# Optimization experiments

Hardware: AMD Instinct MI355X
Metric: run time of the kernel (lower is better)

Reference implementation:

```python
import jax, jax.numpy as jnp
import numpy as np

H = 2048      # hidden_size
NH = 16       # num_heads
HD = H // NH  # head_dim
B, T = 2, 2048


def setup_inputs() -> dict:
    key = jax.random.key(0)
    ks = jax.random.split(key, 5)
    s = 1.0 / np.sqrt(H)
    return {
        "x": jax.random.normal(ks[0], (B, T, H), dtype=jnp.float32),
        "wq": jax.random.normal(ks[1], (H, H), dtype=jnp.float32) * s,
        "bq": jnp.zeros((H,), dtype=jnp.float32),
        "wk": jax.random.normal(ks[2], (H, H), dtype=jnp.float32) * s,
        "bk": jnp.zeros((H,), dtype=jnp.float32),
        "wv": jax.random.normal(ks[3], (H, H), dtype=jnp.float32) * s,
        "bv": jnp.zeros((H,), dtype=jnp.float32),
        "wo": jax.random.normal(ks[4], (H, H), dtype=jnp.float32) * s,
        "bo": jnp.zeros((H,), dtype=jnp.float32),
    }


def reference(x, wq, bq, wk, bk, wv, bv, wo, bo):
    Bx, Tx, C = x.shape
    # projections (torch Linear: x @ W.T + b)
    q = x @ wq.T + bq
    k = x @ wk.T + bk
    v = x @ wv.T + bv
    # [B, T, H] -> [B, NH, T, HD]
    q = q.reshape(Bx, Tx, NH, HD).transpose(0, 2, 1, 3)
    k = k.reshape(Bx, Tx, NH, HD).transpose(0, 2, 1, 3)
    v = v.reshape(Bx, Tx, NH, HD).transpose(0, 2, 1, 3)
    scale = 1.0 / np.sqrt(HD).astype(np.float32)
    scores = jnp.einsum('bhqd,bhkd->bhqk', q, k) * scale  # [B, NH, T, T]
    causal = jnp.tril(jnp.ones((Tx, Tx), dtype=bool))
    scores = jnp.where(causal[None, None], scores, -jnp.inf)
    attn = jax.nn.softmax(scores, axis=-1)
    out = jnp.einsum('bhqk,bhkd->bhqd', attn, v)  # [B, NH, T, HD]
    out = out.transpose(0, 2, 1, 3).reshape(Bx, Tx, C)
    return out @ wo.T + bo
```

## Files before the change

### kernel.cpp

```cpp
#include <hip/hip_runtime.h>
#include <stdint.h>

constexpr int H_  = 2048;
constexpr int NH_ = 16;
constexpr int HD_ = 128;
constexpr int B_  = 2;
constexpr int T_  = 2048;
constexpr int M_  = B_ * T_;

typedef unsigned short u16;
typedef __bf16 bf16x8 __attribute__((ext_vector_type(8)));
typedef float  f32x4  __attribute__((ext_vector_type(4)));

__device__ __forceinline__ u16 f2bf(float f) {
  uint32_t u = __builtin_bit_cast(uint32_t, f);
  u += 0x7fffu + ((u >> 16) & 1u);
  return (u16)(u >> 16);
}

__device__ __forceinline__ void gload_lds16(const void* g, void* lds) {
  auto gp = (const __attribute__((address_space(1))) uint32_t*)(uintptr_t)g;
  auto lp = (__attribute__((address_space(3))) uint32_t*)(uint32_t)(uintptr_t)lds;
  __builtin_amdgcn_global_load_lds(gp, lp, 16, 0, 0);
}

__device__ __forceinline__ f32x4 mfma16(bf16x8 a, bf16x8 b, f32x4 c) {
  return __builtin_amdgcn_mfma_f32_16x16x32_bf16(a, b, c, 0, 0, 0);
}

__global__ __launch_bounds__(512) void cvt5_kernel(
    const float4* __restrict__ x,  const float4* __restrict__ wq,
    const float4* __restrict__ wk, const float4* __restrict__ wv,
    const float4* __restrict__ wo, ushort4* __restrict__ dst) {
  const int bid = blockIdx.x, tid = threadIdx.x;
  const float4* src;
  size_t idx, dof;
  if (bid < 4096) {
    src = x; idx = (size_t)bid * 512 + tid; dof = 0;
  } else {
    int w = (bid - 4096) >> 11;
    int r = (bid - 4096) & 2047;
    idx = (size_t)r * 512 + tid;
    dof = 2097152u + (size_t)w * 1048576u;
    src = (w == 0) ? wq : (w == 1) ? wk : (w == 2) ? wv : wo;
  }
  float4 v = src[idx];
  ushort4 o;
  o.x = f2bf(v.x); o.y = f2bf(v.y); o.z = f2bf(v.z); o.w = f2bf(v.w);
  dst[dof + idx] = o;
}

template <int OUTMODE>
__global__ __launch_bounds__(256) void gemm_bt(const u16* __restrict__ A,
                                               const u16* __restrict__ Bm,
                                               const float* __restrict__ bias,
                                               void* __restrict__ Cout,
                                               int M, int N, int K) {
  __shared__ u16 As[2][128 * 64];
  __shared__ u16 Bs[2][128 * 64];
  const int tid = threadIdx.x;
  const int wave = tid >> 6, lane = tid & 63, l15 = lane & 15, lhi = lane >> 4;
  const int tm = blockIdx.x % (M >> 7), tn = blockIdx.x / (M >> 7);
  const int m0 = tm << 7, n0 = tn << 7;
  const int wr = wave >> 1, wc = wave & 1;
  const int NT = K >> 6;

  f32x4 acc[4][4] = {};

  auto stage = [&](int kt, int buf) {
#pragma unroll
    for (int is = 0; is < 4; ++is) {
      int o  = is * 4096 + tid * 16;
      int row = o >> 7;
      int sw  = o ^ (((o >> 7) & 7) << 4);
      int c8  = (sw >> 4) & 7;
      gload_lds16(A + (size_t)(m0 + row) * K + kt * 64 + c8 * 8,
                  &As[buf][0] + (is * 2048 + wave * 512));
      gload_lds16(Bm + (size_t)(n0 + row) * K + kt * 64 + c8 * 8,
                  &Bs[buf][0] + (is * 2048 + wave * 512));
    }
  };

  stage(0, 0);
  int cur = 0;
  for (int kt = 0; kt < NT; ++kt) {
    if (kt + 1 < NT) {
      stage(kt + 1, cur ^ 1);
      asm volatile("s_waitcnt vmcnt(8)" ::: "memory");
    } else {
      asm volatile("s_waitcnt vmcnt(0)" ::: "memory");
    }
    __builtin_amdgcn_s_barrier();
    asm volatile("" ::: "memory");
#pragma unroll
    for (int kk = 0; kk < 2; ++kk) {
      bf16x8 af[4], bfr[4];
#pragma unroll
      for (int mi = 0; mi < 4; ++mi) {
        int row = wr * 64 + mi * 16 + l15;
        int ob  = (row * 128 + kk * 64 + lhi * 16) ^ ((row & 7) << 4);
        af[mi] = *(const bf16x8*)((const char*)&As[cur][0] + ob);
      }
#pragma unroll
      for (int ni = 0; ni < 4; ++ni) {
        int row = wc * 64 + ni * 16 + l15;
        int ob  = (row * 128 + kk * 64 + lhi * 16) ^ ((row & 7) << 4);
        bfr[ni] = *(const bf16x8*)((const char*)&Bs[cur][0] + ob);
      }
#pragma unroll
      for (int mi = 0; mi < 4; ++mi)
#pragma unroll
        for (int ni = 0; ni < 4; ++ni)
          acc[mi][ni] = mfma16(af[mi], bfr[ni], acc[mi][ni]);
    }
    __builtin_amdgcn_s_barrier();
    asm volatile("" ::: "memory");
    cur ^= 1;
  }

  float bv[4];
#pragma unroll
  for (int ni = 0; ni < 4; ++ni) bv[ni] = bias[n0 + wc * 64 + ni * 16 + l15];

  if constexpr (OUTMODE == 2) {
    const int b = m0 >> 11;
    const int tbase = (m0 & 2047) + wr * 64 + lhi * 4;
#pragma unroll
    for (int mi = 0; mi < 4; ++mi) {
#pragma unroll
      for (int ni = 0; ni < 4; ++ni) {
        int n = n0 + wc * 64 + ni * 16 + l15;
        ushort4 pk;
        pk.x = f2bf(acc[mi][ni][0] + bv[ni]);
        pk.y = f2bf(acc[mi][ni][1] + bv[ni]);
        pk.z = f2bf(acc[mi][ni][2] + bv[ni]);
        pk.w = f2bf(acc[mi][ni][3] + bv[ni]);
        *(ushort4*)((u16*)Cout + (size_t)(b * 2048 + n) * T_ + tbase +
                    mi * 16) = pk;
      }
    }
  } else {
#pragma unroll
    for (int mi = 0; mi < 4; ++mi) {
#pragma unroll
      for (int ni = 0; ni < 4; ++ni) {
        int n = n0 + wc * 64 + ni * 16 + l15;
#pragma unroll
        for (int r = 0; r < 4; ++r) {
          int m = m0 + wr * 64 + mi * 16 + lhi * 4 + r;
          float v = acc[mi][ni][r] + bv[ni];
          if (OUTMODE == 1)
            ((float*)Cout)[(size_t)m * N + n] = v;
          else
            ((u16*)Cout)[(size_t)m * N + n] = f2bf(v);
        }
      }
    }
  }
}

__global__ __launch_bounds__(256) void attn_kernel(const u16* __restrict__ Q,
                                                   const u16* __restrict__ K,
                                                   const u16* __restrict__ Vt,
                                                   u16* __restrict__ ctx) {
  __shared__ u16 Ks[2][64 * 128];
  __shared__ u16 Vs[2][128 * 64];
  __shared__ u16 Ps[4][1024];

  const int tid = threadIdx.x, wave = tid >> 6, lane = tid & 63;
  const int l15 = lane & 15, lhi = lane >> 4;

  const int bid = blockIdx.x;
  const int xcd = bid & 7, idx = bid >> 3;
  const int bh = xcd * 4 + (idx & 3);
  const int qi = idx >> 2;
  const int b = bh >> 4, h = bh & 15;
  const int nQB = T_ / 64;
  const int qbs[2] = {qi, nQB - 1 - qi};

  const float C1  = 0.08838834764831845f * 1.4426950408889634f;
  const float THR = 11.5f;
  const float NI  = -__builtin_inff();

  auto stage = [&](int buf, int kv0) {
#pragma unroll
    for (int is = 0; is < 4; ++is) {
      {
        int o_ = is * 4096 + tid * 16;
        int row = o_ >> 8;
        int sw = o_ ^ (((o_ >> 8) & 7) << 4);
        int c8 = (sw >> 4) & 15;
        gload_lds16(K + (size_t)(b * T_ + kv0 + row) * H_ + h * HD_ + c8 * 8,
                    &Ks[buf][0] + (is * 2048 + wave * 512));
      }
      {
        int o_ = is * 4096 + tid * 16;
        int row = o_ >> 7;
        int sw = o_ ^ (((o_ >> 7) & 7) << 4);
        int t8 = (sw >> 4) & 7;
        gload_lds16(Vt + (size_t)(bh * HD_ + row) * T_ + kv0 + t8 * 8,
                    &Vs[buf][0] + (is * 2048 + wave * 512));
      }
    }
  };

  stage(0, 0);
  asm volatile("s_waitcnt vmcnt(0)" ::: "memory");
  __builtin_amdgcn_s_barrier();
  asm volatile("" ::: "memory");
  int cur = 0;

  for (int s = 0; s < 2; ++s) {
    const int qb = qbs[s];
    const int q0 = qb * 64 + wave * 16;
    const int qrow = q0 + l15;

    bf16x8 qf[4];
    const u16* qbase = Q + (size_t)(b * T_ + q0 + l15) * H_ + h * HD_ + lhi * 8;
#pragma unroll
    for (int kk = 0; kk < 4; ++kk) qf[kk] = *(const bf16x8*)(qbase + kk * 32);

    f32x4 o[8] = {};
    float m2 = NI, lr = 0.f;

    for (int kvb = 0; kvb <= qb; ++kvb) {
      const int kv0 = kvb * 64;
      const bool has_next = (kvb < qb) || (s == 0);
      if (has_next) {
        stage(cur ^ 1, (kvb < qb) ? kv0 + 64 : 0);
        asm volatile("s_waitcnt vmcnt(8)" ::: "memory");
      } else {
        asm volatile("s_waitcnt vmcnt(0)" ::: "memory");
      }
      __builtin_amdgcn_s_barrier();
      asm volatile("" ::: "memory");

      f32x4 sv[4];
      __builtin_amdgcn_s_setprio(1);
#pragma unroll
      for (int kt = 0; kt < 4; ++kt) {
        f32x4 sacc = {0.f, 0.f, 0.f, 0.f};
#pragma unroll
        for (int kk = 0; kk < 4; ++kk) {
          int row = kt * 16 + l15;
          int ob = (row * 256 + kk * 64 + lhi * 16) ^ ((row & 7) << 4);
          bf16x8 kf = *(const bf16x8*)((const char*)&Ks[cur][0] + ob);
          sacc = mfma16(kf, qf[kk], sacc);
        }
        sv[kt] = sacc;
      }
      __builtin_amdgcn_s_setprio(0);

      float pmax2 = NI;
      if (kvb == qb) {
#pragma unroll
        for (int kt = 0; kt < 4; ++kt)
#pragma unroll
          for (int r = 0; r < 4; ++r) {
            int key = kv0 + kt * 16 + lhi * 4 + r;
            float z = sv[kt][r] * C1;
            z = (key <= qrow) ? z : NI;
            sv[kt][r] = z;
            pmax2 = fmaxf(pmax2, z);
          }
      } else {
#pragma unroll
        for (int kt = 0; kt < 4; ++kt)
#pragma unroll
          for (int r = 0; r < 4; ++r) {
            float z = sv[kt][r] * C1;
            sv[kt][r] = z;
            pmax2 = fmaxf(pmax2, z);
          }
      }
      pmax2 = fmaxf(pmax2, __shfl_xor(pmax2, 16));
      pmax2 = fmaxf(pmax2, __shfl_xor(pmax2, 32));

      if (__any(pmax2 - m2 > THR)) {
        float mn = fmaxf(m2, pmax2);
        float al = exp2f(m2 - mn);
        m2 = mn;
        lr *= al;
        float alo[4];
#pragma unroll
        for (int r = 0; r < 4; ++r) alo[r] = __shfl(al, lhi * 4 + r);
#pragma unroll
        for (int dt = 0; dt < 8; ++dt)
#pragma unroll
          for (int r = 0; r < 4; ++r) o[dt][r] *= alo[r];
      }

      float rs = 0.f;
#pragma unroll
      for (int kt = 0; kt < 4; ++kt)
#pragma unroll
        for (int r = 0; r < 4; ++r) {
          float p = exp2f(sv[kt][r] - m2);
          sv[kt][r] = p;
          rs += p;
        }
      rs += __shfl_xor(rs, 16);
      rs += __shfl_xor(rs, 32);
      lr += rs;

#pragma unroll
      for (int kt = 0; kt < 4; ++kt) {
        int slot = kt * 2 + (lhi >> 1);
        ushort4 pk;
        pk.x = f2bf(sv[kt][0]);
        pk.y = f2bf(sv[kt][1]);
        pk.z = f2bf(sv[kt][2]);
        pk.w = f2bf(sv[kt][3]);
        *(ushort4*)&Ps[wave][slot * 128 + ((l15 * 8) ^ ((slot & 7) << 3)) +
                             (lhi & 1) * 4] = pk;
      }
      asm volatile("" ::: "memory");

      __builtin_amdgcn_s_setprio(1);
#pragma unroll
      for (int ks = 0; ks < 2; ++ks) {
        int slot = ks * 4 + lhi;
        bf16x8 pf = *(const bf16x8*)&Ps[wave][slot * 128 +
                                              ((l15 * 8) ^ ((slot & 7) << 3))];
#pragma unroll
        for (int dt = 0; dt < 8; ++dt) {
          int row = dt * 16 + l15;
          int ob = (row * 128 + ks * 64 + lhi * 16) ^ ((row & 7) << 4);
          bf16x8 vf = *(const bf16x8*)((const char*)&Vs[cur][0] + ob);
          o[dt] = mfma16(pf, vf, o[dt]);
        }
      }
      __builtin_amdgcn_s_setprio(0);

      __builtin_amdgcn_s_barrier();
      asm volatile("" ::: "memory");
      cur ^= 1;
    }

    float invo[4];
    {
      float inv = 1.0f / lr;
#pragma unroll
      for (int r = 0; r < 4; ++r) invo[r] = __shfl(inv, lhi * 4 + r);
    }
#pragma unroll
    for (int dt = 0; dt < 8; ++dt)
#pragma unroll
      for (int r = 0; r < 4; ++r) {
        float v = o[dt][r] * invo[r];
        ctx[(size_t)(b * T_ + q0 + lhi * 4 + r) * H_ + h * HD_ + dt * 16 +
            l15] = f2bf(v);
      }
  }
}

extern "C" void kernel_launch(void* const* d_in, const int* in_sizes, int n_in,
                              void* d_out, int out_size, void* d_ws,
                              size_t ws_size, hipStream_t stream) {
  const float* x  = (const float*)d_in[0];
  const float* wq = (const float*)d_in[1];
  const float* bq = (const float*)d_in[2];
  const float* wk = (const float*)d_in[3];
  const float* bk = (const float*)d_in[4];
  const float* wv = (const float*)d_in[5];
  const float* bv = (const float*)d_in[6];
  const float* wo = (const float*)d_in[7];
  const float* bo = (const float*)d_in[8];

  char* ws = (char*)d_ws;
  constexpr size_t SZ_X = (size_t)M_ * H_ * 2;
  constexpr size_t SZ_W = (size_t)H_ * H_ * 2;
  u16* xb  = (u16*)(ws);
  u16* wqb = (u16*)(ws + SZ_X);
  u16* wkb = (u16*)(ws + SZ_X + 1 * SZ_W);
  u16* wvb = (u16*)(ws + SZ_X + 2 * SZ_W);
  u16* wob = (u16*)(ws + SZ_X + 3 * SZ_W);
  u16* Qb  = (u16*)(ws + 1 * SZ_X + 4 * SZ_W);
  u16* Kb  = (u16*)(ws + 2 * SZ_X + 4 * SZ_W);
  u16* Vtb = (u16*)(ws + 3 * SZ_X + 4 * SZ_W);
  u16* ctx = xb;

  cvt5_kernel<<<12288, 512, 0, stream>>>((const float4*)x, (const float4*)wq,
                                         (const float4*)wk, (const float4*)wv,
                                         (const float4*)wo, (ushort4*)ws);

  gemm_bt<0><<<512, 256, 0, stream>>>(xb, wqb, bq, Qb, M_, H_, H_);
  gemm_bt<0><<<512, 256, 0, stream>>>(xb, wkb, bk, Kb, M_, H_, H_);
  gemm_bt<2><<<512, 256, 0, stream>>>(xb, wvb, bv, Vtb, M_, H_, H_);

  attn_kernel<<<512, 256, 0, stream>>>(Qb, Kb, Vtb, ctx);

  gemm_bt<1><<<512, 256, 0, stream>>>(ctx, wob, bo, d_out, M_, H_, H_);
}
```

Baseline: 243.4 us.

## Merge QKV GEMMs into one launch and widen attention blocks to 8 waves

The three QKV projection GEMMs now run as a single 1536-block launch through a shared device function, with the output mode selected at runtime. This removes two launch gaps and lets tail blocks overlap. The attention kernel now uses 512 threads covering 128 query rows per block, so each staged K/V tile is shared by twice as many waves; waves whose rows lie entirely above the causal diagonal skip their compute. P is packed to bf16 with the v_cvt_pk_bf16_f32 instruction. Trade-offs are a runtime outmode branch in the GEMM, half as many attention blocks (256), and idle waves on diagonal tiles.

New measurement: 291.3 us. 19.7% more time.

```diff
diff --git a/kernel.cpp b/kernel.cpp
--- a/kernel.cpp
+++ b/kernel.cpp
@@ -16,6 +16,12 @@
   uint32_t u = __builtin_bit_cast(uint32_t, f);
   u += 0x7fffu + ((u >> 16) & 1u);
   return (u16)(u >> 16);
+}
+
+__device__ __forceinline__ uint32_t cvtpk(float lo, float hi) {
+  uint32_t r;
+  asm("v_cvt_pk_bf16_f32 %0, %1, %2" : "=v"(r) : "v"(lo), "v"(hi));
+  return r;
 }
 
 __device__ __forceinline__ void gload_lds16(const void* g, void* lds) {
@@ -50,20 +56,20 @@
   dst[dof + idx] = o;
 }
 
-template <int OUTMODE>
-__global__ __launch_bounds__(256) void gemm_bt(const u16* __restrict__ A,
-                                               const u16* __restrict__ Bm,
-                                               const float* __restrict__ bias,
-                                               void* __restrict__ Cout,
-                                               int M, int N, int K) {
+__device__ __forceinline__ void gemm_core(const u16* __restrict__ A,
+                                          const u16* __restrict__ Bm,
+                                          const float* __restrict__ bias,
+                                          void* __restrict__ Cout,
+                                          int bid, int outmode) {
   __shared__ u16 As[2][128 * 64];
   __shared__ u16 Bs[2][128 * 64];
+  constexpr int Mg = M_, Ng = H_, Kg = H_;
   const int tid = threadIdx.x;
   const int wave = tid >> 6, lane = tid & 63, l15 = lane & 15, lhi = lane >> 4;
-  const int tm = blockIdx.x % (M >> 7), tn = blockIdx.x / (M >> 7);
+  const int tm = bid % (Mg >> 7), tn = bid / (Mg >> 7);
   const int m0 = tm << 7, n0 = tn << 7;
   const int wr = wave >> 1, wc = wave & 1;
-  const int NT = K >> 6;
+  const int NT = Kg >> 6;
 
   f32x4 acc[4][4] = {};
 
@@ -74,9 +80,9 @@
       int row = o >> 7;
       int sw  = o ^ (((o >> 7) & 7) << 4);
       int c8  = (sw >> 4) & 7;
-      gload_lds16(A + (size_t)(m0 + row) * K + kt * 64 + c8 * 8,
+      gload_lds16(A + (size_t)(m0 + row) * Kg + kt * 64 + c8 * 8,
                   &As[buf][0] + (is * 2048 + wave * 512));
-      gload_lds16(Bm + (size_t)(n0 + row) * K + kt * 64 + c8 * 8,
+      gload_lds16(Bm + (size_t)(n0 + row) * Kg + kt * 64 + c8 * 8,
                   &Bs[buf][0] + (is * 2048 + wave * 512));
     }
   };
@@ -122,7 +128,7 @@
 #pragma unroll
   for (int ni = 0; ni < 4; ++ni) bv[ni] = bias[n0 + wc * 64 + ni * 16 + l15];
 
-  if constexpr (OUTMODE == 2) {
+  if (outmode == 2) {
     const int b = m0 >> 11;
     const int tbase = (m0 & 2047) + wr * 64 + lhi * 4;
 #pragma unroll
@@ -149,23 +155,42 @@
         for (int r = 0; r < 4; ++r) {
           int m = m0 + wr * 64 + mi * 16 + lhi * 4 + r;
           float v = acc[mi][ni][r] + bv[ni];
-          if (OUTMODE == 1)
-            ((float*)Cout)[(size_t)m * N + n] = v;
+          if (outmode == 1)
+            ((float*)Cout)[(size_t)m * Ng + n] = v;
           else
-            ((u16*)Cout)[(size_t)m * N + n] = f2bf(v);
+            ((u16*)Cout)[(size_t)m * Ng + n] = f2bf(v);
         }
       }
     }
   }
 }
 
-__global__ __launch_bounds__(256) void attn_kernel(const u16* __restrict__ Q,
-                                                   const u16* __restrict__ K,
-                                                   const u16* __restrict__ Vt,
-                                                   u16* __restrict__ ctx) {
+__global__ __launch_bounds__(256) void gemm_qkv(
+    const u16* __restrict__ xb, const u16* __restrict__ wqb,
+    const u16* __restrict__ wkb, const u16* __restrict__ wvb,
+    const float* __restrict__ bq, const float* __restrict__ bk,
+    const float* __restrict__ bv, u16* __restrict__ Qb, u16* __restrict__ Kb,
+    u16* __restrict__ Vtb) {
+  const int g = blockIdx.x >> 9, bid = blockIdx.x & 511;
+  const u16* Bm = (g == 0) ? wqb : (g == 1) ? wkb : wvb;
+  const float* bias = (g == 0) ? bq : (g == 1) ? bk : bv;
+  void* out = (g == 0) ? (void*)Qb : (g == 1) ? (void*)Kb : (void*)Vtb;
+  gemm_core(xb, Bm, bias, out, bid, (g == 2) ? 2 : 0);
+}
+
+__global__ __launch_bounds__(256) void gemm_out(const u16* __restrict__ A,
+                                                const u16* __restrict__ Bm,
+                                                const float* __restrict__ bias,
+                                                float* __restrict__ Cout) {
+  gemm_core(A, Bm, bias, Cout, blockIdx.x, 1);
+}
+
+__global__ __launch_bounds__(512, 4) void attn_kernel(
+    const u16* __restrict__ Q, const u16* __restrict__ K,
+    const u16* __restrict__ Vt, u16* __restrict__ ctx) {
   __shared__ u16 Ks[2][64 * 128];
   __shared__ u16 Vs[2][128 * 64];
-  __shared__ u16 Ps[4][1024];
+  __shared__ u16 Ps[8][1024];
 
   const int tid = threadIdx.x, wave = tid >> 6, lane = tid & 63;
   const int l15 = lane & 15, lhi = lane >> 4;
@@ -173,10 +198,9 @@
   const int bid = blockIdx.x;
   const int xcd = bid & 7, idx = bid >> 3;
   const int bh = xcd * 4 + (idx & 3);
-  const int qi = idx >> 2;
+  const int pj = idx >> 2;
   const int b = bh >> 4, h = bh & 15;
-  const int nQB = T_ / 64;
-  const int qbs[2] = {qi, nQB - 1 - qi};
+  const int qts[2] = {pj, 15 - pj};
 
   const float C1  = 0.08838834764831845f * 1.4426950408889634f;
   const float THR = 11.5f;
@@ -184,22 +208,22 @@
 
   auto stage = [&](int buf, int kv0) {
 #pragma unroll
-    for (int is = 0; is < 4; ++is) {
+    for (int is = 0; is < 2; ++is) {
       {
-        int o_ = is * 4096 + tid * 16;
+        int o_ = is * 8192 + tid * 16;
         int row = o_ >> 8;
         int sw = o_ ^ (((o_ >> 8) & 7) << 4);
         int c8 = (sw >> 4) & 15;
         gload_lds16(K + (size_t)(b * T_ + kv0 + row) * H_ + h * HD_ + c8 * 8,
-                    &Ks[buf][0] + (is * 2048 + wave * 512));
+                    &Ks[buf][0] + (is * 4096 + wave * 512));
       }
       {
-        int o_ = is * 4096 + tid * 16;
+        int o_ = is * 8192 + tid * 16;
         int row = o_ >> 7;
         int sw = o_ ^ (((o_ >> 7) & 7) << 4);
         int t8 = (sw >> 4) & 7;
         gload_lds16(Vt + (size_t)(bh * HD_ + row) * T_ + kv0 + t8 * 8,
-                    &Vs[buf][0] + (is * 2048 + wave * 512));
+                    &Vs[buf][0] + (is * 4096 + wave * 512));
       }
     }
   };
@@ -211,9 +235,10 @@
   int cur = 0;
 
   for (int s = 0; s < 2; ++s) {
-    const int qb = qbs[s];
-    const int q0 = qb * 64 + wave * 16;
+    const int qt = qts[s];
+    const int q0 = qt * 128 + wave * 16;
     const int qrow = q0 + l15;
+    const int nkv = 2 * qt + 2;
 
     bf16x8 qf[4];
     const u16* qbase = Q + (size_t)(b * T_ + q0 + l15) * H_ + h * HD_ + lhi * 8;
@@ -223,114 +248,114 @@
     f32x4 o[8] = {};
     float m2 = NI, lr = 0.f;
 
-    for (int kvb = 0; kvb <= qb; ++kvb) {
+    for (int kvb = 0; kvb < nkv; ++kvb) {
       const int kv0 = kvb * 64;
-      const bool has_next = (kvb < qb) || (s == 0);
+      const bool has_next = (kvb + 1 < nkv) || (s == 0);
       if (has_next) {
-        stage(cur ^ 1, (kvb < qb) ? kv0 + 64 : 0);
-        asm volatile("s_waitcnt vmcnt(8)" ::: "memory");
+        stage(cur ^ 1, (kvb + 1 < nkv) ? kv0 + 64 : 0);
+        asm volatile("s_waitcnt vmcnt(4)" ::: "memory");
       } else {
         asm volatile("s_waitcnt vmcnt(0)" ::: "memory");
       }
       __builtin_amdgcn_s_barrier();
       asm volatile("" ::: "memory");
 
-      f32x4 sv[4];
-      __builtin_amdgcn_s_setprio(1);
-#pragma unroll
-      for (int kt = 0; kt < 4; ++kt) {
-        f32x4 sacc = {0.f, 0.f, 0.f, 0.f};
-#pragma unroll
-        for (int kk = 0; kk < 4; ++kk) {
-          int row = kt * 16 + l15;
-          int ob = (row * 256 + kk * 64 + lhi * 16) ^ ((row & 7) << 4);
-          bf16x8 kf = *(const bf16x8*)((const char*)&Ks[cur][0] + ob);
-          sacc = mfma16(kf, qf[kk], sacc);
-        }
-        sv[kt] = sacc;
-      }
-      __builtin_amdgcn_s_setprio(0);
-
-      float pmax2 = NI;
-      if (kvb == qb) {
+      if (kv0 <= q0 + 15) {
+        f32x4 sv[4];
+        __builtin_amdgcn_s_setprio(1);
+#pragma unroll
+        for (int kt = 0; kt < 4; ++kt) {
+          f32x4 sacc = {0.f, 0.f, 0.f, 0.f};
+#pragma unroll
+          for (int kk = 0; kk < 4; ++kk) {
+            int row = kt * 16 + l15;
+            int ob = (row * 256 + kk * 64 + lhi * 16) ^ ((row & 7) << 4);
+            bf16x8 kf = *(const bf16x8*)((const char*)&Ks[cur][0] + ob);
+            sacc = mfma16(kf, qf[kk], sacc);
+          }
+          sv[kt] = sacc;
+        }
+        __builtin_amdgcn_s_setprio(0);
+
+        float pmax2 = NI;
+        if (kv0 + 63 > q0) {
+#pragma unroll
+          for (int kt = 0; kt < 4; ++kt)
+#pragma unroll
+            for (int r = 0; r < 4; ++r) {
+              int key = kv0 + kt * 16 + lhi * 4 + r;
+              float z = sv[kt][r] * C1;
+              z = (key <= qrow) ? z : NI;
+              sv[kt][r] = z;
+              pmax2 = fmaxf(pmax2, z);
+            }
+        } else {
+#pragma unroll
+          for (int kt = 0; kt < 4; ++kt)
+#pragma unroll
+            for (int r = 0; r < 4; ++r) {
+              float z = sv[kt][r] * C1;
+              sv[kt][r] = z;
+              pmax2 = fmaxf(pmax2, z);
+            }
+        }
+        pmax2 = fmaxf(pmax2, __shfl_xor(pmax2, 16));
+        pmax2 = fmaxf(pmax2, __shfl_xor(pmax2, 32));
+
+        if (__any(pmax2 - m2 > THR)) {
+          float mn = fmaxf(m2, pmax2);
+          float al = exp2f(m2 - mn);
+          m2 = mn;
+          lr *= al;
+          float alo[4];
+#pragma unroll
+          for (int r = 0; r < 4; ++r) alo[r] = __shfl(al, lhi * 4 + r);
+#pragma unroll
+          for (int dt = 0; dt < 8; ++dt)
+#pragma unroll
+            for (int r = 0; r < 4; ++r) o[dt][r] *= alo[r];
+        }
+
+        float rs = 0.f;
 #pragma unroll
         for (int kt = 0; kt < 4; ++kt)
 #pragma unroll
           for (int r = 0; r < 4; ++r) {
-            int key = kv0 + kt * 16 + lhi * 4 + r;
-            float z = sv[kt][r] * C1;
-            z = (key <= qrow) ? z : NI;
-            sv[kt][r] = z;
-            pmax2 = fmaxf(pmax2, z);
+            float p = exp2f(sv[kt][r] - m2);
+            sv[kt][r] = p;
+            rs += p;
           }
-      } else {
-#pragma unroll
-        for (int kt = 0; kt < 4; ++kt)
-#pragma unroll
-          for (int r = 0; r < 4; ++r) {
-            float z = sv[kt][r] * C1;
-            sv[kt][r] = z;
-            pmax2 = fmaxf(pmax2, z);
+        rs += __shfl_xor(rs, 16);
+        rs += __shfl_xor(rs, 32);
+        lr += rs;
+
+#pragma unroll
+        for (int kt = 0; kt < 4; ++kt) {
+          int slot = kt * 2 + (lhi >> 1);
+          uint2 pk;
+          pk.x = cvtpk(sv[kt][0], sv[kt][1]);
+          pk.y = cvtpk(sv[kt][2], sv[kt][3]);
+          *(uint2*)&Ps[wave][slot * 128 + ((l15 * 8) ^ ((slot & 7) << 3)) +
+                             (lhi & 1) * 4] = pk;
+        }
+        asm volatile("" ::: "memory");
+
+        __builtin_amdgcn_s_setprio(1);
+#pragma unroll
+        for (int ks = 0; ks < 2; ++ks) {
+          int slot = ks * 4 + lhi;
+          bf16x8 pf = *(const bf16x8*)&Ps[wave][slot * 128 + ((l15 * 8) ^
+                                                             ((slot & 7) << 3))];
+#pragma unroll
+          for (int dt = 0; dt < 8; ++dt) {
+            int row = dt * 16 + l15;
+            int ob = (row * 128 + ks * 64 + lhi * 16) ^ ((row & 7) << 4);
+            bf16x8 vf = *(const bf16x8*)((const char*)&Vs[cur][0] + ob);
+            o[dt] = mfma16(pf, vf, o[dt]);
           }
-      }
-      pmax2 = fmaxf(pmax2, __shfl_xor(pmax2, 16));
-      pmax2 = fmaxf(pmax2, __shfl_xor(pmax2, 32));
-
-      if (__any(pmax2 - m2 > THR)) {
-        float mn = fmaxf(m2, pmax2);
-        float al = exp2f(m2 - mn);
-        m2 = mn;
-        lr *= al;
-        float alo[4];
-#pragma unroll
-        for (int r = 0; r < 4; ++r) alo[r] = __shfl(al, lhi * 4 + r);
-#pragma unroll
-        for (int dt = 0; dt < 8; ++dt)
-#pragma unroll
-          for (int r = 0; r < 4; ++r) o[dt][r] *= alo[r];
-      }
-
-      float rs = 0.f;
-#pragma unroll
-      for (int kt = 0; kt < 4; ++kt)
-#pragma unroll
-        for (int r = 0; r < 4; ++r) {
-          float p = exp2f(sv[kt][r] - m2);
-          sv[kt][r] = p;
-          rs += p;
-        }
-      rs += __shfl_xor(rs, 16);
-      rs += __shfl_xor(rs, 32);
-      lr += rs;
-
-#pragma unroll
-      for (int kt = 0; kt < 4; ++kt) {
-        int slot = kt * 2 + (lhi >> 1);
-        ushort4 pk;
-        pk.x = f2bf(sv[kt][0]);
-        pk.y = f2bf(sv[kt][1]);
-        pk.z = f2bf(sv[kt][2]);
-        pk.w = f2bf(sv[kt][3]);
-        *(ushort4*)&Ps[wave][slot * 128 + ((l15 * 8) ^ ((slot & 7) << 3)) +
-                             (lhi & 1) * 4] = pk;
-      }
-      asm volatile("" ::: "memory");
-
-      __builtin_amdgcn_s_setprio(1);
-#pragma unroll
-      for (int ks = 0; ks < 2; ++ks) {
-        int slot = ks * 4 + lhi;
-        bf16x8 pf = *(const bf16x8*)&Ps[wave][slot * 128 +
-                                              ((l15 * 8) ^ ((slot & 7) << 3))];
-#pragma unroll
-        for (int dt = 0; dt < 8; ++dt) {
-          int row = dt * 16 + l15;
-          int ob = (row * 128 + ks * 64 + lhi * 16) ^ ((row & 7) << 4);
-          bf16x8 vf = *(const bf16x8*)((const char*)&Vs[cur][0] + ob);
-          o[dt] = mfma16(pf, vf, o[dt]);
-        }
-      }
-      __builtin_amdgcn_s_setprio(0);
+        }
+        __builtin_amdgcn_s_setprio(0);
+      }
 
       __builtin_amdgcn_s_barrier();
       asm volatile("" ::: "memory");
@@ -384,11 +409,10 @@
                                          (const float4*)wk, (const float4*)wv,
                                          (const float4*)wo, (ushort4*)ws);
 
-  gemm_bt<0><<<512, 256, 0, stream>>>(xb, wqb, bq, Qb, M_, H_, H_);
-  gemm_bt<0><<<512, 256, 0, stream>>>(xb, wkb, bk, Kb, M_, H_, H_);
-  gemm_bt<2><<<512, 256, 0, stream>>>(xb, wvb, bv, Vtb, M_, H_, H_);
-
-  attn_kernel<<<512, 256, 0, stream>>>(Qb, Kb, Vtb, ctx);
-
-  gemm_bt<1><<<512, 256, 0, stream>>>(ctx, wob, bo, d_out, M_, H_, H_);
-}
+  gemm_qkv<<<1536, 256, 0, stream>>>(xb, wqb, wkb, wvb, bq, bk, bv, Qb, Kb,
+                                     Vtb);
+
+  attn_kernel<<<256, 512, 0, stream>>>(Qb, Kb, Vtb, ctx);
+
+  gemm_out<<<512, 256, 0, stream>>>(ctx, wob, bo, (float*)d_out);
+}
```
